# Kernel optimization log

Hardware: AMD Instinct MI355X
Metric: run time of the kernel (lower is better)

## Reference

```python
import jax, jax.numpy as jnp
import numpy as np

B, S, HID = 2, 2048, 2048
NH, NKV = 16, 4
HD = HID // NH            # 128
N_REP = NH // NKV          # 4
THETA = 10000.0
NEG = -1e9


def _rope_tables(position_ids):
    # inv_freq: [HD/2]
    inv_freq = 1.0 / (THETA ** (jnp.arange(0, HD, 2, dtype=jnp.float32) / HD))
    freqs = position_ids.astype(jnp.float32)[..., None] * inv_freq  # [B,S,HD/2]
    emb = jnp.concatenate([freqs, freqs], axis=-1)                  # [B,S,HD]
    return jnp.cos(emb), jnp.sin(emb)


def _rotate_half(x):
    return jnp.concatenate([-x[..., HD // 2:], x[..., :HD // 2]], axis=-1)


def setup_inputs() -> dict:
    key = jax.random.key(0)
    k1, k2, k3 = jax.random.split(key, 3)
    hidden_states = jax.random.normal(k1, (B, S, HID), dtype=jnp.float32)
    w_qkv = jax.random.normal(k2, (HID + 2 * NKV * HD, HID), dtype=jnp.float32) * 0.02
    w_out = jax.random.normal(k3, (HID, HID), dtype=jnp.float32) * 0.02
    causal = jnp.tril(jnp.ones((S, S), dtype=bool))
    attention_mask = jnp.where(causal, 0.0, NEG).astype(jnp.float32)
    attention_mask = jnp.broadcast_to(attention_mask[None, None], (B, 1, S, S))
    position_ids = jnp.broadcast_to(jnp.arange(S, dtype=jnp.int64), (B, S))
    return {"hidden_states": hidden_states, "w_qkv": w_qkv, "w_out": w_out,
            "attention_mask": attention_mask, "position_ids": position_ids}


def reference(hidden_states, w_qkv, w_out, attention_mask, position_ids):
    bsz, q_len, _ = hidden_states.shape
    qkv = hidden_states @ w_qkv.T                                   # [B,S,HID+2*NKV*HD]
    q, k, v = jnp.split(qkv, [HID, HID + NKV * HD], axis=-1)
    q = q.reshape(bsz, q_len, NH, HD).transpose(0, 2, 1, 3)         # [B,NH,S,HD]
    k = k.reshape(bsz, q_len, NKV, HD).transpose(0, 2, 1, 3)        # [B,NKV,S,HD]
    v = v.reshape(bsz, q_len, NKV, HD).transpose(0, 2, 1, 3)

    cos, sin = _rope_tables(position_ids)                           # [B,S,HD]
    cos, sin = cos[:, None], sin[:, None]                           # unsqueeze head dim
    q = q * cos + _rotate_half(q) * sin
    k = k * cos + _rotate_half(k) * sin

    # GQA: repeat KV heads to match query heads (repeat_kv)
    k = jnp.repeat(k, N_REP, axis=1)                                # [B,NH,S,HD]
    v = jnp.repeat(v, N_REP, axis=1)

    scale = 1.0 / jnp.sqrt(jnp.float32(HD))
    scores = jnp.einsum('bhqd,bhkd->bhqk', q, k) * scale
    scores = scores + attention_mask                                # [B,NH,S,S]
    attn = jax.nn.softmax(scores.astype(jnp.float32), axis=-1).astype(q.dtype)
    out = jnp.einsum('bhqk,bhkd->bhqd', attn, v)                    # [B,NH,S,HD]
    out = out.transpose(0, 2, 1, 3).reshape(bsz, q_len, HID)
    return out @ w_out.T
```

## Files before the change

kernel.cpp:

```cpp
#include <hip/hip_runtime.h>
#include <hip/hip_bf16.h>
#include <math.h>

#define S_LEN   2048
#define HIDDEN  2048
#define NHEADS  16
#define NKVH    4
#define HDIM    128

typedef short  short8  __attribute__((ext_vector_type(8)));
typedef float  floatx4 __attribute__((ext_vector_type(4)));
typedef __hip_bfloat16 bf16;

__device__ inline void async_copy16(const void* g, void* l) {
  __builtin_amdgcn_global_load_lds((__attribute__((address_space(1))) void*)(g),
                                   (__attribute__((address_space(3))) void*)(l),
                                   16, 0, 0);
}

__device__ inline unsigned short cvt1(float x) {
  bf16 t = __float2bfloat16(x);
  return *reinterpret_cast<unsigned short*>(&t);
}
__device__ inline float us2f(unsigned short u) {
  unsigned int v = ((unsigned int)u) << 16;
  return *reinterpret_cast<float*>(&v);
}

#define N8_H  1048576
#define N8_WQ  786432
#define N8_WO  524288
__global__ __launch_bounds__(256) void cvt_all(const float* __restrict__ h,
                                               const float* __restrict__ wq,
                                               const float* __restrict__ wo,
                                               unsigned short* __restrict__ dst) {
  const int i = blockIdx.x * 256 + threadIdx.x;
  if (i >= N8_H + N8_WQ + N8_WO) return;
  const float* src; int j;
  if (i < N8_H)              { src = h;  j = i; }
  else if (i < N8_H + N8_WQ) { src = wq; j = i - N8_H; }
  else                       { src = wo; j = i - N8_H - N8_WQ; }
  const float4 a = reinterpret_cast<const float4*>(src)[j * 2];
  const float4 b = reinterpret_cast<const float4*>(src)[j * 2 + 1];
  unsigned short o[8] = {cvt1(a.x), cvt1(a.y), cvt1(a.z), cvt1(a.w),
                         cvt1(b.x), cvt1(b.y), cvt1(b.z), cvt1(b.w)};
  *reinterpret_cast<short8*>(dst + (size_t)i * 8) = *reinterpret_cast<short8*>(o);
}

template<int MODE>
__global__ __launch_bounds__(512, 2) void gemm8(const bf16* __restrict__ A,
                                                const bf16* __restrict__ B,
                                                bf16* __restrict__ qbuf,
                                                bf16* __restrict__ kbuf,
                                                bf16* __restrict__ vtbuf,
                                                float* __restrict__ Cout)
{
  constexpr int K      = 2048;
  constexpr int BM     = (MODE == 0) ? 256 : 128;
  constexpr int BN     = 256;
  constexpr int MF     = BM / 32;
  constexpr int AI     = BM / 128;
  constexpr int ABYTES = BM * 64;
  constexpr int SLOT   = (BM + BN) * 64;
  constexpr int NSTEP  = K / 32;

  __shared__ __align__(16) unsigned short smem[SLOT * 4 / 2];
  char* smb = (char*)smem;

  const int bn = blockIdx.x, bm = blockIdx.y;
  const int t = threadIdx.x, w = t >> 6, lane = t & 63;
  const int m16 = lane & 15, quad = lane >> 4;
  const int wmr = (w >> 2) * (BM / 2);
  const int wn  = w & 3;

  int bcol[4];
#pragma unroll
  for (int ni = 0; ni < 4; ++ni)
    bcol[ni] = (MODE == 0)
             ? ((wn >> 1) * 128 + (wn & 1) * 32 + (ni & 1) * 16 + (ni >> 1) * 64)
             : (wn * 64 + ni * 16);

  int afo[MF], bfo[4];
#pragma unroll
  for (int mf = 0; mf < MF; ++mf) {
    const int r = wmr + mf * 16 + m16;
    afo[mf] = r * 64 + ((quad ^ ((r >> 1) & 3)) << 4);
  }
#pragma unroll
  for (int ni = 0; ni < 4; ++ni) {
    const int r = bcol[ni] + m16;
    bfo[ni] = ABYTES + r * 64 + ((quad ^ ((r >> 1) & 3)) << 4);
  }

  const bf16* srcA[AI]; int dstA[AI];
#pragma unroll
  for (int j = 0; j < AI; ++j) {
    const int ci  = w * AI + j;
    const int row = ci * 16 + (lane >> 2);
    const int sl  = (lane & 3) ^ ((row >> 1) & 3);
    srcA[j] = A + (size_t)(bm * BM + row) * K + sl * 8;
    dstA[j] = ci * 1024;
  }
  const bf16* srcB[2]; int dstB[2];
#pragma unroll
  for (int j = 0; j < 2; ++j) {
    const int ci  = w * 2 + j;
    const int row = ci * 16 + (lane >> 2);
    const int sl  = (lane & 3) ^ ((row >> 1) & 3);
    srcB[j] = B + (size_t)(bn * BN + row) * K + sl * 8;
    dstB[j] = ABYTES + ci * 1024;
  }

  auto stage = [&](int step, int slotbyte) {
#pragma unroll
    for (int j = 0; j < AI; ++j)
      async_copy16(srcA[j] + step * 32, smb + slotbyte + dstA[j]);
#pragma unroll
    for (int j = 0; j < 2; ++j)
      async_copy16(srcB[j] + step * 32, smb + slotbyte + dstB[j]);
  };

  const floatx4 zf = {0.f, 0.f, 0.f, 0.f};
  floatx4 acc[MF][4];
#pragma unroll
  for (int mf = 0; mf < MF; ++mf)
#pragma unroll
    for (int ni = 0; ni < 4; ++ni) acc[mf][ni] = zf;

  stage(0, 0); stage(1, SLOT); stage(2, 2 * SLOT);

#pragma unroll 4
  for (int s = 0; s < NSTEP; ++s) {
    __builtin_amdgcn_sched_barrier(0);
    if constexpr (MODE == 0) asm volatile("s_waitcnt vmcnt(8)" ::: "memory");
    else                     asm volatile("s_waitcnt vmcnt(6)" ::: "memory");
    __builtin_amdgcn_s_barrier();
    __builtin_amdgcn_sched_barrier(0);
    const int sb  = (s & 3) * SLOT;
    const int ns  = (s + 3) & (NSTEP - 1);
    const int nsb = ((s + 3) & 3) * SLOT;
    if constexpr (MODE == 0) {
      short8 bfr[4], afA[4];
#pragma unroll
      for (int ni = 0; ni < 4; ++ni)
        bfr[ni] = *reinterpret_cast<const short8*>(smb + sb + bfo[ni]);
#pragma unroll
      for (int mf = 0; mf < 4; ++mf)
        afA[mf] = *reinterpret_cast<const short8*>(smb + sb + afo[mf]);
#pragma unroll
      for (int j = 0; j < AI; ++j)
        async_copy16(srcA[j] + ns * 32, smb + nsb + dstA[j]);
      asm volatile("s_waitcnt lgkmcnt(0)" ::: "memory");
      __builtin_amdgcn_sched_barrier(0);
      __builtin_amdgcn_s_setprio(1);
#pragma unroll
      for (int mf = 0; mf < 4; ++mf)
#pragma unroll
        for (int ni = 0; ni < 4; ++ni)
          acc[mf][ni] = __builtin_amdgcn_mfma_f32_16x16x32_bf16(afA[mf], bfr[ni], acc[mf][ni], 0, 0, 0);
      __builtin_amdgcn_s_setprio(0);
      __builtin_amdgcn_s_barrier();
      short8 afB[4];
#pragma unroll
      for (int mf = 0; mf < 4; ++mf)
        afB[mf] = *reinterpret_cast<const short8*>(smb + sb + afo[4 + mf]);
#pragma unroll
      for (int j = 0; j < 2; ++j)
        async_copy16(srcB[j] + ns * 32, smb + nsb + dstB[j]);
      asm volatile("s_waitcnt lgkmcnt(0)" ::: "memory");
      __builtin_amdgcn_sched_barrier(0);
      __builtin_amdgcn_s_setprio(1);
#pragma unroll
      for (int mf = 0; mf < 4; ++mf)
#pragma unroll
        for (int ni = 0; ni < 4; ++ni)
          acc[4 + mf][ni] = __builtin_amdgcn_mfma_f32_16x16x32_bf16(afB[mf], bfr[ni], acc[4 + mf][ni], 0, 0, 0);
      __builtin_amdgcn_s_setprio(0);
    } else {
      short8 af[MF], bfr[4];
#pragma unroll
      for (int mf = 0; mf < MF; ++mf)
        af[mf] = *reinterpret_cast<const short8*>(smb + sb + afo[mf]);
#pragma unroll
      for (int ni = 0; ni < 4; ++ni)
        bfr[ni] = *reinterpret_cast<const short8*>(smb + sb + bfo[ni]);
      stage(ns, nsb);
      __builtin_amdgcn_s_setprio(1);
#pragma unroll
      for (int mf = 0; mf < MF; ++mf)
#pragma unroll
        for (int ni = 0; ni < 4; ++ni)
          acc[mf][ni] = __builtin_amdgcn_mfma_f32_16x16x32_bf16(af[mf], bfr[ni], acc[mf][ni], 0, 0, 0);
      __builtin_amdgcn_s_setprio(0);
    }
  }
  __builtin_amdgcn_s_waitcnt(0);

  if constexpr (MODE == 1) {
#pragma unroll
    for (int mf = 0; mf < MF; ++mf)
#pragma unroll
      for (int ni = 0; ni < 4; ++ni) {
        const int row0 = bm * BM + wmr + mf * 16 + quad * 4;
        const int col  = bn * BN + bcol[ni] + m16;
#pragma unroll
        for (int r = 0; r < 4; ++r)
          Cout[(size_t)(row0 + r) * HIDDEN + col] = acc[mf][ni][r];
      }
  } else {
    const int colbase = bn * BN;
    if (colbase < HIDDEN + NKVH * HDIM) {
      const bool isQ = (colbase < HIDDEN);
      const float post = isQ ? 0.08838834764831845f : 1.0f;
      float invf[2];
#pragma unroll
      for (int p = 0; p < 2; ++p)
        invf[p] = exp2f((float)((wn & 1) * 32 + p * 16 + m16) * -0.2076205059f);
#pragma unroll
      for (int mf = 0; mf < MF; ++mf) {
        const int row0 = bm * BM + wmr + mf * 16 + quad * 4;
#pragma unroll
        for (int r = 0; r < 4; ++r) {
          const int m = row0 + r;
          const int b = m >> 11, s = m & 2047;
          float sn[2], cs[2];
          __sincosf((float)s * invf[0], &sn[0], &cs[0]);
          __sincosf((float)s * invf[1], &sn[1], &cs[1]);
#pragma unroll
          for (int ni = 0; ni < 4; ++ni) {
            const int p = ni & 1;
            const float v  = acc[mf][ni][r];
            const float v2 = acc[mf][ni ^ 2][r];
            const float rot = ((ni < 2) ? (v * cs[p] - v2 * sn[p])
                                        : (v * cs[p] + v2 * sn[p])) * post;
            const int col = colbase + bcol[ni] + m16;
            if (isQ) {
              const int hh = col >> 7, d = col & 127;
              qbuf[(((size_t)(b * NHEADS + hh)) * S_LEN + s) * HDIM + d] = __float2bfloat16(rot);
            } else {
              const int nn = col - HIDDEN; const int hh = nn >> 7, d = nn & 127;
              kbuf[(((size_t)(b * NKVH + hh)) * S_LEN + s) * HDIM + d] = __float2bfloat16(rot);
            }
          }
        }
      }
    } else {
#pragma unroll
      for (int mf = 0; mf < MF; ++mf)
#pragma unroll
        for (int ni = 0; ni < 4; ++ni) {
          const int col = colbase + bcol[ni] + m16;
          const int nn = col - HIDDEN - NKVH * HDIM;
          const int hh = nn >> 7, d = nn & 127;
          const int row0 = bm * BM + wmr + mf * 16 + quad * 4;
#pragma unroll
          for (int r = 0; r < 4; ++r) {
            const int m = row0 + r;
            const int b = m >> 11, s = m & 2047;
            vtbuf[(((size_t)(b * NKVH + hh)) * HDIM + d) * S_LEN + s] =
                __float2bfloat16(acc[mf][ni][r]);
          }
        }
    }
  }
}

__global__ __launch_bounds__(256) void attn_partial(const bf16* __restrict__ qbuf,
                                                    const bf16* __restrict__ kbuf,
                                                    const bf16* __restrict__ vtbuf,
                                                    unsigned short* __restrict__ pnum,
                                                    float* __restrict__ plsum,
                                                    bf16* __restrict__ abuf)
{
  __shared__ unsigned short Ks[4][4096];
  __shared__ unsigned short Vs[4][4096];
  __shared__ unsigned short Ps[4][1280];
  const int sidx = 110 - blockIdx.x;
  int i2, c, nch;
  if (sidx < 27)      { i2 = sidx;                     c = 0;              nch = 1; }
  else if (sidx < 81) { i2 = 27 + ((sidx - 27) >> 1);  c = (sidx - 27) & 1; nch = 2; }
  else                { i2 = 54 + (sidx - 81) / 3;     c = (sidx - 81) % 3; nch = 3; }
  const int len = i2 + 1;
  const int k0 = (c * len) / nch, k1 = ((c + 1) * len) / nch;
  const int kvh = blockIdx.y, b = blockIdx.z;
  const int t = threadIdx.x, w = t >> 6, lane = t & 63;
  const int m16 = lane & 15, quad = lane >> 4;
  const int h = kvh * 4 + w;

  const bf16* Qp = qbuf + (((size_t)(b * NHEADS + h)) * S_LEN + i2 * 32 + m16) * HDIM;
  short8 qf[2][4];
#pragma unroll
  for (int T = 0; T < 2; ++T)
#pragma unroll
    for (int cc = 0; cc < 4; ++cc)
      qf[T][cc] = *reinterpret_cast<const short8*>(Qp + (size_t)T * 16 * HDIM + cc * 32 + quad * 8);

  const bf16* Kp  = kbuf  + ((size_t)(b * NKVH + kvh)) * S_LEN * HDIM;
  const bf16* Vtp = vtbuf + ((size_t)(b * NKVH + kvh)) * HDIM * S_LEN;

  const int kk = lane >> 4, cK = lane & 15;
  const int rKa = w * 8 + kk, rKb = rKa + 4;
  const int offKa = rKa * 128 + ((cK ^ (rKa & 7)) * 8);
  const int offKb = rKb * 128 + ((cK ^ (rKb & 7)) * 8);
  const int dd = lane >> 2, cV = lane & 3;
  const int dVa = w * 32 + dd, dVb = dVa + 16;
  const int offVa = dVa * 2048 + ((cV ^ ((dVa >> 1) & 3)) * 8);
  const int offVb = dVb * 2048 + ((cV ^ ((dVb >> 1) & 3)) * 8);

  const floatx4 zf = {0.f, 0.f, 0.f, 0.f};
  floatx4 oacc[2][8];
#pragma unroll
  for (int T = 0; T < 2; ++T)
#pragma unroll
    for (int d = 0; d < 8; ++d) oacc[T][d] = zf;
  floatx4 lacc[2] = {zf, zf};
  unsigned short ones_s[8] = {0x3F80,0x3F80,0x3F80,0x3F80,0x3F80,0x3F80,0x3F80,0x3F80};
  const short8 ones = *reinterpret_cast<short8*>(ones_s);

  unsigned short* Pw = &Ps[w][0];

  auto stage_tile = [&](int kt) {
    const int sl = kt & 3;
    const int ks = kt * 32;
    async_copy16(Kp + (size_t)ks * 128 + offKa, &Ks[sl][w * 1024]);
    async_copy16(Kp + (size_t)ks * 128 + offKb, &Ks[sl][w * 1024 + 512]);
    async_copy16(Vtp + ks + offVa, &Vs[sl][w * 1024]);
    async_copy16(Vtp + ks + offVb, &Vs[sl][w * 1024 + 512]);
  };

  auto qk = [&](int kt, floatx4& s00, floatx4& s01, floatx4& s10, floatx4& s11) {
    const int sl = kt & 3;
    s00 = zf; s01 = zf; s10 = zf; s11 = zf;
#pragma unroll
    for (int cc = 0; cc < 4; ++cc) {
      const int sw = ((cc * 4 + quad) ^ (m16 & 7)) * 8;
      short8 kf0 = *reinterpret_cast<const short8*>(&Ks[sl][m16 * 128 + sw]);
      short8 kf1 = *reinterpret_cast<const short8*>(&Ks[sl][(16 + m16) * 128 + sw]);
      s00 = __builtin_amdgcn_mfma_f32_16x16x32_bf16(qf[0][cc], kf0, s00, 0, 0, 0);
      s01 = __builtin_amdgcn_mfma_f32_16x16x32_bf16(qf[0][cc], kf1, s01, 0, 0, 0);
      s10 = __builtin_amdgcn_mfma_f32_16x16x32_bf16(qf[1][cc], kf0, s10, 0, 0, 0);
      s11 = __builtin_amdgcn_mfma_f32_16x16x32_bf16(qf[1][cc], kf1, s11, 0, 0, 0);
    }
  };

  auto finish = [&](int kt, const floatx4& s00, const floatx4& s01,
                    const floatx4& s10, const floatx4& s11) {
    const int sl = kt & 3;
    const int ks = kt * 32;
#pragma unroll
    for (int T = 0; T < 2; ++T) {
      const floatx4& sa = T ? s10 : s00;
      const floatx4& sb = T ? s11 : s01;
#pragma unroll
      for (int r = 0; r < 4; ++r) {
        const int row = i2 * 32 + T * 16 + quad * 4 + r;
        const float p0 = (ks + m16      > row) ? 0.f : __expf(sa[r]);
        const float p1 = (ks + 16 + m16 > row) ? 0.f : __expf(sb[r]);
        Pw[(T * 16 + quad * 4 + r) * 40 + m16]      = cvt1(p0);
        Pw[(T * 16 + quad * 4 + r) * 40 + 16 + m16] = cvt1(p1);
      }
    }
    const short8 pa0 = *reinterpret_cast<const short8*>(&Pw[m16 * 40 + quad * 8]);
    const short8 pa1 = *reinterpret_cast<const short8*>(&Pw[(16 + m16) * 40 + quad * 8]);
    lacc[0] = __builtin_amdgcn_mfma_f32_16x16x32_bf16(pa0, ones, lacc[0], 0, 0, 0);
    lacc[1] = __builtin_amdgcn_mfma_f32_16x16x32_bf16(pa1, ones, lacc[1], 0, 0, 0);
#pragma unroll
    for (int dt = 0; dt < 8; ++dt) {
      short8 vfr = *reinterpret_cast<const short8*>(
          &Vs[sl][(dt * 16 + m16) * 32 + ((quad ^ ((m16 >> 1) & 3)) * 8)]);
      oacc[0][dt] = __builtin_amdgcn_mfma_f32_16x16x32_bf16(pa0, vfr, oacc[0][dt], 0, 0, 0);
      oacc[1][dt] = __builtin_amdgcn_mfma_f32_16x16x32_bf16(pa1, vfr, oacc[1][dt], 0, 0, 0);
    }
  };

  stage_tile(k0);
  if (k0 + 1 < k1) stage_tile(k0 + 1);
  __syncthreads();
  floatx4 a00, a01, a10, a11, b00, b01, b10, b11;
  qk(k0, a00, a01, a10, a11);

  int ki = k0 + 1;
  for (; ki + 1 < k1; ki += 2) {
    stage_tile(ki + 1);
    qk(ki, b00, b01, b10, b11);
    finish(ki - 1, a00, a01, a10, a11);
    __syncthreads();
    if (ki + 2 < k1) stage_tile(ki + 2);
    qk(ki + 1, a00, a01, a10, a11);
    finish(ki, b00, b01, b10, b11);
    __syncthreads();
  }
  if (ki < k1) {
    qk(ki, b00, b01, b10, b11);
    finish(ki - 1, a00, a01, a10, a11);
    finish(ki, b00, b01, b10, b11);
  } else {
    finish(ki - 1, a00, a01, a10, a11);
  }

  if (nch == 1) {
#pragma unroll
    for (int T = 0; T < 2; ++T) {
      float invl[4];
#pragma unroll
      for (int r = 0; r < 4; ++r) invl[r] = 1.0f / lacc[T][r];
      bf16* op = abuf + (((size_t)b * S_LEN + i2 * 32 + T * 16 + quad * 4) * NHEADS + h) * HDIM + m16;
#pragma unroll
      for (int dt = 0; dt < 8; ++dt)
#pragma unroll
        for (int r = 0; r < 4; ++r)
          op[(size_t)r * NHEADS * HDIM + dt * 16] = __float2bfloat16(oacc[T][dt][r] * invl[r]);
    }
  } else {
    const int b0 = (i2 < 54) ? (27 + 2 * (i2 - 27)) : (81 + 3 * (i2 - 54));
    const int slot = (b * NHEADS + h) * 111 + b0 + c;
    unsigned short* np = pnum + (size_t)slot * 4096;
#pragma unroll
    for (int T = 0; T < 2; ++T)
#pragma unroll
      for (int dt = 0; dt < 8; ++dt)
#pragma unroll
        for (int r = 0; r < 4; ++r)
          np[(T * 16 + quad * 4 + r) * 128 + dt * 16 + m16] = cvt1(oacc[T][dt][r]);
    if (m16 == 0) {
#pragma unroll
      for (int T = 0; T < 2; ++T)
#pragma unroll
        for (int r = 0; r < 4; ++r)
          plsum[slot * 32 + T * 16 + quad * 4 + r] = lacc[T][r];
    }
  }
}

__global__ __launch_bounds__(256) void attn_combine(const unsigned short* __restrict__ pnum,
                                                    const float* __restrict__ plsum,
                                                    bf16* __restrict__ abuf)
{
  const int i = 54 + blockIdx.x;
  const int h = blockIdx.y, b = blockIdx.z;
  const int i2 = i >> 1, lr0 = (i & 1) * 16;
  const int t = threadIdx.x, row16 = t >> 4, c0 = (t & 15) * 8;
  const int lr = lr0 + row16;
  const int nch = (i2 < 54) ? 2 : 3;
  const int b0  = (i2 < 54) ? (27 + 2 * (i2 - 27)) : (81 + 3 * (i2 - 54));
  const int hb = (b * NHEADS + h) * 111 + b0;
  float acc[8] = {0.f,0.f,0.f,0.f,0.f,0.f,0.f,0.f};
  float lsum = 0.f;
  for (int c = 0; c < nch; ++c) {
    const unsigned short* np = pnum + (size_t)(hb + c) * 4096 + lr * 128 + c0;
    const short8 v = *reinterpret_cast<const short8*>(np);
#pragma unroll
    for (int j = 0; j < 8; ++j) acc[j] += us2f(((unsigned short*)&v)[j]);
    lsum += plsum[(hb + c) * 32 + lr];
  }
  const float invl = 1.0f / lsum;
  unsigned short o[8];
#pragma unroll
  for (int j = 0; j < 8; ++j) o[j] = cvt1(acc[j] * invl);
  *reinterpret_cast<short8*>(abuf + (((size_t)b * S_LEN + i * 16 + row16) * NHEADS + h) * HDIM + c0)
      = *reinterpret_cast<short8*>(o);
}

extern "C" void kernel_launch(void* const* d_in, const int* in_sizes, int n_in,
                              void* d_out, int out_size, void* d_ws, size_t ws_size,
                              hipStream_t stream) {
  const float* hidden_f = (const float*)d_in[0];
  const float* wqkv_f   = (const float*)d_in[1];
  const float* wout_f   = (const float*)d_in[2];
  float* out = (float*)d_out;

  char* ws = (char*)d_ws;
  bf16* hbf    = (bf16*)(ws);
  bf16* wqkvbf = (bf16*)(ws + 16777216);
  bf16* woutbf = (bf16*)(ws + 29360128);
  bf16* qbuf   = (bf16*)(ws + 37748736);
  bf16* kbuf   = (bf16*)(ws + 54525952);
  bf16* vtbuf  = (bf16*)(ws + 58720256);
  bf16* abuf   = (bf16*)(ws + 62914560);
  unsigned short* pnum = (unsigned short*)(ws);
  float* plsum = (float*)(ws + 79691776);

  cvt_all<<<9216, 256, 0, stream>>>(hidden_f, wqkv_f, wout_f, (unsigned short*)ws);

  gemm8<0><<<dim3(12, 16), 512, 0, stream>>>(hbf, wqkvbf, qbuf, kbuf, vtbuf, nullptr);
  attn_partial<<<dim3(111, 4, 2), 256, 0, stream>>>(qbuf, kbuf, vtbuf, pnum, plsum, abuf);
  attn_combine<<<dim3(74, 16, 2), 256, 0, stream>>>(pnum, plsum, abuf);
  gemm8<1><<<dim3(8, 32), 512, 0, stream>>>(abuf, woutbf, nullptr, nullptr, nullptr, out);
}
```

Baseline: 303.5 us.

## Use 32x32x16 MFMA in attention and keep P in registers via lane shuffles

```diff
diff --git a/kernel.cpp b/kernel.cpp
--- a/kernel.cpp
+++ b/kernel.cpp
@@ -8,8 +8,10 @@
 #define NKVH    4
 #define HDIM    128
 
-typedef short  short8  __attribute__((ext_vector_type(8)));
-typedef float  floatx4 __attribute__((ext_vector_type(4)));
+typedef short  short8   __attribute__((ext_vector_type(8)));
+typedef float  floatx4  __attribute__((ext_vector_type(4)));
+typedef float  floatx16 __attribute__((ext_vector_type(16)));
+typedef int    intx4    __attribute__((ext_vector_type(4)));
 typedef __hip_bfloat16 bf16;
 
 __device__ inline void async_copy16(const void* g, void* l) {
@@ -274,7 +276,6 @@
 {
   __shared__ unsigned short Ks[4][4096];
   __shared__ unsigned short Vs[4][4096];
-  __shared__ unsigned short Ps[4][1280];
   const int sidx = 110 - blockIdx.x;
   int i2, c, nch;
   if (sidx < 27)      { i2 = sidx;                     c = 0;              nch = 1; }
@@ -284,40 +285,32 @@
   const int k0 = (c * len) / nch, k1 = ((c + 1) * len) / nch;
   const int kvh = blockIdx.y, b = blockIdx.z;
   const int t = threadIdx.x, w = t >> 6, lane = t & 63;
-  const int m16 = lane & 15, quad = lane >> 4;
+  const int l31 = lane & 31, hi = lane >> 5;
   const int h = kvh * 4 + w;
 
-  const bf16* Qp = qbuf + (((size_t)(b * NHEADS + h)) * S_LEN + i2 * 32 + m16) * HDIM;
-  short8 qf[2][4];
-#pragma unroll
-  for (int T = 0; T < 2; ++T)
-#pragma unroll
-    for (int cc = 0; cc < 4; ++cc)
-      qf[T][cc] = *reinterpret_cast<const short8*>(Qp + (size_t)T * 16 * HDIM + cc * 32 + quad * 8);
+  const bf16* Qp = qbuf + (((size_t)(b * NHEADS + h)) * S_LEN + i2 * 32 + l31) * HDIM;
+  short8 qf[8];
+#pragma unroll
+  for (int cc = 0; cc < 8; ++cc)
+    qf[cc] = *reinterpret_cast<const short8*>(Qp + cc * 16 + hi * 8);
 
   const bf16* Kp  = kbuf  + ((size_t)(b * NKVH + kvh)) * S_LEN * HDIM;
   const bf16* Vtp = vtbuf + ((size_t)(b * NKVH + kvh)) * HDIM * S_LEN;
 
   const int kk = lane >> 4, cK = lane & 15;
   const int rKa = w * 8 + kk, rKb = rKa + 4;
-  const int offKa = rKa * 128 + ((cK ^ (rKa & 7)) * 8);
-  const int offKb = rKb * 128 + ((cK ^ (rKb & 7)) * 8);
+  const int offKa = rKa * 128 + ((cK ^ (rKa & 15)) * 8);
+  const int offKb = rKb * 128 + ((cK ^ (rKb & 15)) * 8);
   const int dd = lane >> 2, cV = lane & 3;
   const int dVa = w * 32 + dd, dVb = dVa + 16;
   const int offVa = dVa * 2048 + ((cV ^ ((dVa >> 1) & 3)) * 8);
   const int offVb = dVb * 2048 + ((cV ^ ((dVb >> 1) & 3)) * 8);
 
-  const floatx4 zf = {0.f, 0.f, 0.f, 0.f};
-  floatx4 oacc[2][8];
-#pragma unroll
-  for (int T = 0; T < 2; ++T)
-#pragma unroll
-    for (int d = 0; d < 8; ++d) oacc[T][d] = zf;
-  floatx4 lacc[2] = {zf, zf};
+  floatx16 oacc[4], lacc;
+#pragma unroll
+  for (int i = 0; i < 16; ++i) { lacc[i] = 0.f; oacc[0][i] = 0.f; oacc[1][i] = 0.f; oacc[2][i] = 0.f; oacc[3][i] = 0.f; }
   unsigned short ones_s[8] = {0x3F80,0x3F80,0x3F80,0x3F80,0x3F80,0x3F80,0x3F80,0x3F80};
   const short8 ones = *reinterpret_cast<short8*>(ones_s);
-
-  unsigned short* Pw = &Ps[w][0];
 
   auto stage_tile = [&](int kt) {
     const int sl = kt & 3;
@@ -328,106 +321,108 @@
     async_copy16(Vtp + ks + offVb, &Vs[sl][w * 1024 + 512]);
   };
 
-  auto qk = [&](int kt, floatx4& s00, floatx4& s01, floatx4& s10, floatx4& s11) {
+  auto qk = [&](int kt, floatx16& s) {
     const int sl = kt & 3;
-    s00 = zf; s01 = zf; s10 = zf; s11 = zf;
-#pragma unroll
-    for (int cc = 0; cc < 4; ++cc) {
-      const int sw = ((cc * 4 + quad) ^ (m16 & 7)) * 8;
-      short8 kf0 = *reinterpret_cast<const short8*>(&Ks[sl][m16 * 128 + sw]);
-      short8 kf1 = *reinterpret_cast<const short8*>(&Ks[sl][(16 + m16) * 128 + sw]);
-      s00 = __builtin_amdgcn_mfma_f32_16x16x32_bf16(qf[0][cc], kf0, s00, 0, 0, 0);
-      s01 = __builtin_amdgcn_mfma_f32_16x16x32_bf16(qf[0][cc], kf1, s01, 0, 0, 0);
-      s10 = __builtin_amdgcn_mfma_f32_16x16x32_bf16(qf[1][cc], kf0, s10, 0, 0, 0);
-      s11 = __builtin_amdgcn_mfma_f32_16x16x32_bf16(qf[1][cc], kf1, s11, 0, 0, 0);
+#pragma unroll
+    for (int i = 0; i < 16; ++i) s[i] = 0.f;
+#pragma unroll
+    for (int cc = 0; cc < 8; ++cc) {
+      const short8 kf = *reinterpret_cast<const short8*>(
+          &Ks[sl][l31 * 128 + (((cc * 2 + hi) ^ (l31 & 15)) * 8)]);
+      s = __builtin_amdgcn_mfma_f32_32x32x16_bf16(kf, qf[cc], s, 0, 0, 0);
     }
   };
 
-  auto finish = [&](int kt, const floatx4& s00, const floatx4& s01,
-                    const floatx4& s10, const floatx4& s11) {
+  auto finish = [&](int kt, const floatx16& s) {
     const int sl = kt & 3;
     const int ks = kt * 32;
-#pragma unroll
-    for (int T = 0; T < 2; ++T) {
-      const floatx4& sa = T ? s10 : s00;
-      const floatx4& sb = T ? s11 : s01;
-#pragma unroll
-      for (int r = 0; r < 4; ++r) {
-        const int row = i2 * 32 + T * 16 + quad * 4 + r;
-        const float p0 = (ks + m16      > row) ? 0.f : __expf(sa[r]);
-        const float p1 = (ks + 16 + m16 > row) ? 0.f : __expf(sb[r]);
-        Pw[(T * 16 + quad * 4 + r) * 40 + m16]      = cvt1(p0);
-        Pw[(T * 16 + quad * 4 + r) * 40 + 16 + m16] = cvt1(p1);
-      }
-    }
-    const short8 pa0 = *reinterpret_cast<const short8*>(&Pw[m16 * 40 + quad * 8]);
-    const short8 pa1 = *reinterpret_cast<const short8*>(&Pw[(16 + m16) * 40 + quad * 8]);
-    lacc[0] = __builtin_amdgcn_mfma_f32_16x16x32_bf16(pa0, ones, lacc[0], 0, 0, 0);
-    lacc[1] = __builtin_amdgcn_mfma_f32_16x16x32_bf16(pa1, ones, lacc[1], 0, 0, 0);
-#pragma unroll
-    for (int dt = 0; dt < 8; ++dt) {
-      short8 vfr = *reinterpret_cast<const short8*>(
-          &Vs[sl][(dt * 16 + m16) * 32 + ((quad ^ ((m16 >> 1) & 3)) * 8)]);
-      oacc[0][dt] = __builtin_amdgcn_mfma_f32_16x16x32_bf16(pa0, vfr, oacc[0][dt], 0, 0, 0);
-      oacc[1][dt] = __builtin_amdgcn_mfma_f32_16x16x32_bf16(pa1, vfr, oacc[1][dt], 0, 0, 0);
+    const int qrow = i2 * 32 + l31;
+    unsigned int cw[8];
+#pragma unroll
+    for (int tt = 0; tt < 8; ++tt) {
+      const int r0 = 2 * tt;
+      const int key0 = ks + (r0 & 3) + 8 * (r0 >> 2) + 4 * hi;
+      const float p0 = (key0     > qrow) ? 0.f : __expf(s[r0]);
+      const float p1 = (key0 + 1 > qrow) ? 0.f : __expf(s[r0 + 1]);
+      cw[tt] = ((unsigned int)cvt1(p1) << 16) | cvt1(p0);
+    }
+    unsigned int pc[8];
+#pragma unroll
+    for (int tt = 0; tt < 8; ++tt) pc[tt] = (unsigned int)__shfl_xor((int)cw[tt], 32);
+    intx4 f0, f1;
+    f0[0] = (int)(hi ? pc[2] : cw[0]); f0[1] = (int)(hi ? pc[3] : cw[1]);
+    f0[2] = (int)(hi ? cw[2] : pc[0]); f0[3] = (int)(hi ? cw[3] : pc[1]);
+    f1[0] = (int)(hi ? pc[6] : cw[4]); f1[1] = (int)(hi ? pc[7] : cw[5]);
+    f1[2] = (int)(hi ? cw[6] : pc[4]); f1[3] = (int)(hi ? cw[7] : pc[5]);
+    const short8 pf0 = __builtin_bit_cast(short8, f0);
+    const short8 pf1 = __builtin_bit_cast(short8, f1);
+    lacc = __builtin_amdgcn_mfma_f32_32x32x16_bf16(pf0, ones, lacc, 0, 0, 0);
+    lacc = __builtin_amdgcn_mfma_f32_32x32x16_bf16(pf1, ones, lacc, 0, 0, 0);
+#pragma unroll
+    for (int db = 0; db < 4; ++db) {
+      const int drow = db * 32 + l31;
+      const int xr = (drow >> 1) & 3;
+      const short8 vf0 = *reinterpret_cast<const short8*>(
+          &Vs[sl][drow * 32 + ((hi ^ xr) * 8)]);
+      oacc[db] = __builtin_amdgcn_mfma_f32_32x32x16_bf16(pf0, vf0, oacc[db], 0, 0, 0);
+      const short8 vf1 = *reinterpret_cast<const short8*>(
+          &Vs[sl][drow * 32 + (((2 + hi) ^ xr) * 8)]);
+      oacc[db] = __builtin_amdgcn_mfma_f32_32x32x16_bf16(pf1, vf1, oacc[db], 0, 0, 0);
     }
   };
 
   stage_tile(k0);
   if (k0 + 1 < k1) stage_tile(k0 + 1);
   __syncthreads();
-  floatx4 a00, a01, a10, a11, b00, b01, b10, b11;
-  qk(k0, a00, a01, a10, a11);
+  floatx16 sa, sb;
+  qk(k0, sa);
 
   int ki = k0 + 1;
   for (; ki + 1 < k1; ki += 2) {
     stage_tile(ki + 1);
-    qk(ki, b00, b01, b10, b11);
-    finish(ki - 1, a00, a01, a10, a11);
+    qk(ki, sb);
+    finish(ki - 1, sa);
     __syncthreads();
     if (ki + 2 < k1) stage_tile(ki + 2);
-    qk(ki + 1, a00, a01, a10, a11);
-    finish(ki, b00, b01, b10, b11);
+    qk(ki + 1, sa);
+    finish(ki, sb);
     __syncthreads();
   }
   if (ki < k1) {
-    qk(ki, b00, b01, b10, b11);
-    finish(ki - 1, a00, a01, a10, a11);
-    finish(ki, b00, b01, b10, b11);
+    qk(ki, sb);
+    finish(ki - 1, sa);
+    finish(ki, sb);
   } else {
-    finish(ki - 1, a00, a01, a10, a11);
+    finish(ki - 1, sa);
   }
 
   if (nch == 1) {
-#pragma unroll
-    for (int T = 0; T < 2; ++T) {
-      float invl[4];
-#pragma unroll
-      for (int r = 0; r < 4; ++r) invl[r] = 1.0f / lacc[T][r];
-      bf16* op = abuf + (((size_t)b * S_LEN + i2 * 32 + T * 16 + quad * 4) * NHEADS + h) * HDIM + m16;
-#pragma unroll
-      for (int dt = 0; dt < 8; ++dt)
-#pragma unroll
-        for (int r = 0; r < 4; ++r)
-          op[(size_t)r * NHEADS * HDIM + dt * 16] = __float2bfloat16(oacc[T][dt][r] * invl[r]);
-    }
+    float invl[16];
+#pragma unroll
+    for (int r = 0; r < 16; ++r) invl[r] = 1.0f / lacc[r];
+#pragma unroll
+    for (int db = 0; db < 4; ++db)
+#pragma unroll
+      for (int r = 0; r < 16; ++r) {
+        const int row = i2 * 32 + (r & 3) + 8 * (r >> 2) + 4 * hi;
+        abuf[(((size_t)b * S_LEN + row) * NHEADS + h) * HDIM + db * 32 + l31] =
+            __float2bfloat16(oacc[db][r] * invl[r]);
+      }
   } else {
     const int b0 = (i2 < 54) ? (27 + 2 * (i2 - 27)) : (81 + 3 * (i2 - 54));
     const int slot = (b * NHEADS + h) * 111 + b0 + c;
     unsigned short* np = pnum + (size_t)slot * 4096;
 #pragma unroll
-    for (int T = 0; T < 2; ++T)
-#pragma unroll
-      for (int dt = 0; dt < 8; ++dt)
-#pragma unroll
-        for (int r = 0; r < 4; ++r)
-          np[(T * 16 + quad * 4 + r) * 128 + dt * 16 + m16] = cvt1(oacc[T][dt][r]);
-    if (m16 == 0) {
-#pragma unroll
-      for (int T = 0; T < 2; ++T)
-#pragma unroll
-        for (int r = 0; r < 4; ++r)
-          plsum[slot * 32 + T * 16 + quad * 4 + r] = lacc[T][r];
+    for (int db = 0; db < 4; ++db)
+#pragma unroll
+      for (int r = 0; r < 16; ++r) {
+        const int row = (r & 3) + 8 * (r >> 2) + 4 * hi;
+        np[row * 128 + db * 32 + l31] = cvt1(oacc[db][r]);
+      }
+    if (l31 == 0) {
+#pragma unroll
+      for (int r = 0; r < 16; ++r)
+        plsum[slot * 32 + (r & 3) + 8 * (r >> 2) + 4 * hi] = lacc[r];
     }
   }
 }
```

New measurement: 328.3 us. +8.1%, slower.

## Stage 128-key K/V blocks per sync and rebalance split-K chunk partitioning

Applied to the files above, without the earlier changes.

```diff
diff --git a/kernel.cpp b/kernel.cpp
--- a/kernel.cpp
+++ b/kernel.cpp
@@ -272,16 +272,16 @@
                                                     float* __restrict__ plsum,
                                                     bf16* __restrict__ abuf)
 {
-  __shared__ unsigned short Ks[4][4096];
-  __shared__ unsigned short Vs[4][4096];
+  __shared__ unsigned short Ks[16384];
+  __shared__ unsigned short Vs[16384];
   __shared__ unsigned short Ps[4][1280];
-  const int sidx = 110 - blockIdx.x;
+  const int sidx = 119 - blockIdx.x;
   int i2, c, nch;
-  if (sidx < 27)      { i2 = sidx;                     c = 0;              nch = 1; }
-  else if (sidx < 81) { i2 = 27 + ((sidx - 27) >> 1);  c = (sidx - 27) & 1; nch = 2; }
-  else                { i2 = 54 + (sidx - 81) / 3;     c = (sidx - 81) % 3; nch = 3; }
-  const int len = i2 + 1;
-  const int k0 = (c * len) / nch, k1 = ((c + 1) * len) / nch;
+  if (sidx < 24)      { i2 = sidx;                          c = 0;     nch = 1; }
+  else if (sidx < 72) { const int q = sidx - 24; i2 = 24 + (q >> 1); c = q & 1; nch = 2; }
+  else                { const int q = sidx - 72; i2 = 48 + q / 3;    c = q % 3; nch = 3; }
+  const int L = (i2 >> 2) + 1;
+  const int kb0 = (c * L) / nch, kb1 = ((c + 1) * L) / nch;
   const int kvh = blockIdx.y, b = blockIdx.z;
   const int t = threadIdx.x, w = t >> 6, lane = t & 63;
   const int m16 = lane & 15, quad = lane >> 4;
@@ -298,14 +298,8 @@
   const bf16* Kp  = kbuf  + ((size_t)(b * NKVH + kvh)) * S_LEN * HDIM;
   const bf16* Vtp = vtbuf + ((size_t)(b * NKVH + kvh)) * HDIM * S_LEN;
 
-  const int kk = lane >> 4, cK = lane & 15;
-  const int rKa = w * 8 + kk, rKb = rKa + 4;
-  const int offKa = rKa * 128 + ((cK ^ (rKa & 7)) * 8);
-  const int offKb = rKb * 128 + ((cK ^ (rKb & 7)) * 8);
-  const int dd = lane >> 2, cV = lane & 3;
-  const int dVa = w * 32 + dd, dVb = dVa + 16;
-  const int offVa = dVa * 2048 + ((cV ^ ((dVa >> 1) & 3)) * 8);
-  const int offVb = dVb * 2048 + ((cV ^ ((dVb >> 1) & 3)) * 8);
+  const int ls = lane >> 4;
+  const int lc = lane & 15;
 
   const floatx4 zf = {0.f, 0.f, 0.f, 0.f};
   floatx4 oacc[2][8];
@@ -319,23 +313,24 @@
 
   unsigned short* Pw = &Ps[w][0];
 
-  auto stage_tile = [&](int kt) {
-    const int sl = kt & 3;
-    const int ks = kt * 32;
-    async_copy16(Kp + (size_t)ks * 128 + offKa, &Ks[sl][w * 1024]);
-    async_copy16(Kp + (size_t)ks * 128 + offKb, &Ks[sl][w * 1024 + 512]);
-    async_copy16(Vtp + ks + offVa, &Vs[sl][w * 1024]);
-    async_copy16(Vtp + ks + offVb, &Vs[sl][w * 1024 + 512]);
+  auto stage_tile = [&](int kb) {
+#pragma unroll
+    for (int j = 0; j < 8; ++j) {
+      const int r = w * 32 + j * 4 + ls;
+      async_copy16(Kp + ((size_t)(kb * 128 + r)) * 128 + ((lc ^ (r & 7)) * 8),
+                   &Ks[(w * 32 + j * 4) * 128]);
+      async_copy16(Vtp + (size_t)r * 2048 + kb * 128 + ((lc ^ (r & 7)) * 8),
+                   &Vs[(w * 32 + j * 4) * 128]);
+    }
   };
 
-  auto qk = [&](int kt, floatx4& s00, floatx4& s01, floatx4& s10, floatx4& s11) {
-    const int sl = kt & 3;
+  auto qk = [&](int sub, floatx4& s00, floatx4& s01, floatx4& s10, floatx4& s11) {
     s00 = zf; s01 = zf; s10 = zf; s11 = zf;
 #pragma unroll
     for (int cc = 0; cc < 4; ++cc) {
-      const int sw = ((cc * 4 + quad) ^ (m16 & 7)) * 8;
-      short8 kf0 = *reinterpret_cast<const short8*>(&Ks[sl][m16 * 128 + sw]);
-      short8 kf1 = *reinterpret_cast<const short8*>(&Ks[sl][(16 + m16) * 128 + sw]);
+      const int ch = ((cc * 4 + quad) ^ (m16 & 7)) * 8;
+      short8 kf0 = *reinterpret_cast<const short8*>(&Ks[(sub * 32 + m16) * 128 + ch]);
+      short8 kf1 = *reinterpret_cast<const short8*>(&Ks[(sub * 32 + 16 + m16) * 128 + ch]);
       s00 = __builtin_amdgcn_mfma_f32_16x16x32_bf16(qf[0][cc], kf0, s00, 0, 0, 0);
       s01 = __builtin_amdgcn_mfma_f32_16x16x32_bf16(qf[0][cc], kf1, s01, 0, 0, 0);
       s10 = __builtin_amdgcn_mfma_f32_16x16x32_bf16(qf[1][cc], kf0, s10, 0, 0, 0);
@@ -343,10 +338,9 @@
     }
   };
 
-  auto finish = [&](int kt, const floatx4& s00, const floatx4& s01,
+  auto finish = [&](int kb, int sub, const floatx4& s00, const floatx4& s01,
                     const floatx4& s10, const floatx4& s11) {
-    const int sl = kt & 3;
-    const int ks = kt * 32;
+    const int ks = kb * 128 + sub * 32;
 #pragma unroll
     for (int T = 0; T < 2; ++T) {
       const floatx4& sa = T ? s10 : s00;
@@ -367,35 +361,35 @@
 #pragma unroll
     for (int dt = 0; dt < 8; ++dt) {
       short8 vfr = *reinterpret_cast<const short8*>(
-          &Vs[sl][(dt * 16 + m16) * 32 + ((quad ^ ((m16 >> 1) & 3)) * 8)]);
+          &Vs[(dt * 16 + m16) * 128 + (((sub * 4 + quad) ^ (m16 & 7)) * 8)]);
       oacc[0][dt] = __builtin_amdgcn_mfma_f32_16x16x32_bf16(pa0, vfr, oacc[0][dt], 0, 0, 0);
       oacc[1][dt] = __builtin_amdgcn_mfma_f32_16x16x32_bf16(pa1, vfr, oacc[1][dt], 0, 0, 0);
     }
   };
 
-  stage_tile(k0);
-  if (k0 + 1 < k1) stage_tile(k0 + 1);
-  __syncthreads();
-  floatx4 a00, a01, a10, a11, b00, b01, b10, b11;
-  qk(k0, a00, a01, a10, a11);
-
-  int ki = k0 + 1;
-  for (; ki + 1 < k1; ki += 2) {
-    stage_tile(ki + 1);
-    qk(ki, b00, b01, b10, b11);
-    finish(ki - 1, a00, a01, a10, a11);
+  for (int kb = kb0; kb < kb1; ++kb) {
     __syncthreads();
-    if (ki + 2 < k1) stage_tile(ki + 2);
-    qk(ki + 1, a00, a01, a10, a11);
-    finish(ki, b00, b01, b10, b11);
+    stage_tile(kb);
     __syncthreads();
-  }
-  if (ki < k1) {
-    qk(ki, b00, b01, b10, b11);
-    finish(ki - 1, a00, a01, a10, a11);
-    finish(ki, b00, b01, b10, b11);
-  } else {
-    finish(ki - 1, a00, a01, a10, a11);
+    const int rem = i2 - 4 * kb + 1;
+    floatx4 a0, a1, a2, a3, b0, b1, b2, b3;
+    qk(0, a0, a1, a2, a3);
+    if (rem == 1) { finish(kb, 0, a0, a1, a2, a3); }
+    else {
+      qk(1, b0, b1, b2, b3);
+      finish(kb, 0, a0, a1, a2, a3);
+      if (rem == 2) { finish(kb, 1, b0, b1, b2, b3); }
+      else {
+        qk(2, a0, a1, a2, a3);
+        finish(kb, 1, b0, b1, b2, b3);
+        if (rem == 3) { finish(kb, 2, a0, a1, a2, a3); }
+        else {
+          qk(3, b0, b1, b2, b3);
+          finish(kb, 2, a0, a1, a2, a3);
+          finish(kb, 3, b0, b1, b2, b3);
+        }
+      }
+    }
   }
 
   if (nch == 1) {
@@ -412,8 +406,8 @@
           op[(size_t)r * NHEADS * HDIM + dt * 16] = __float2bfloat16(oacc[T][dt][r] * invl[r]);
     }
   } else {
-    const int b0 = (i2 < 54) ? (27 + 2 * (i2 - 27)) : (81 + 3 * (i2 - 54));
-    const int slot = (b * NHEADS + h) * 111 + b0 + c;
+    const int base = (i2 < 48) ? (i2 - 24) * 2 : 48 + (i2 - 48) * 3;
+    const int slot = (b * NHEADS + h) * 96 + base + c;
     unsigned short* np = pnum + (size_t)slot * 4096;
 #pragma unroll
     for (int T = 0; T < 2; ++T)
@@ -436,14 +430,14 @@
                                                     const float* __restrict__ plsum,
                                                     bf16* __restrict__ abuf)
 {
-  const int i = 54 + blockIdx.x;
+  const int i = blockIdx.x;
+  const int i2 = 24 + (i >> 1), lr0 = (i & 1) * 16;
   const int h = blockIdx.y, b = blockIdx.z;
-  const int i2 = i >> 1, lr0 = (i & 1) * 16;
   const int t = threadIdx.x, row16 = t >> 4, c0 = (t & 15) * 8;
   const int lr = lr0 + row16;
-  const int nch = (i2 < 54) ? 2 : 3;
-  const int b0  = (i2 < 54) ? (27 + 2 * (i2 - 27)) : (81 + 3 * (i2 - 54));
-  const int hb = (b * NHEADS + h) * 111 + b0;
+  const int nch  = (i2 < 48) ? 2 : 3;
+  const int base = (i2 < 48) ? (i2 - 24) * 2 : 48 + (i2 - 48) * 3;
+  const int hb = (b * NHEADS + h) * 96 + base;
   float acc[8] = {0.f,0.f,0.f,0.f,0.f,0.f,0.f,0.f};
   float lsum = 0.f;
   for (int c = 0; c < nch; ++c) {
@@ -457,7 +451,7 @@
   unsigned short o[8];
 #pragma unroll
   for (int j = 0; j < 8; ++j) o[j] = cvt1(acc[j] * invl);
-  *reinterpret_cast<short8*>(abuf + (((size_t)b * S_LEN + i * 16 + row16) * NHEADS + h) * HDIM + c0)
+  *reinterpret_cast<short8*>(abuf + (((size_t)b * S_LEN + i2 * 32 + lr) * NHEADS + h) * HDIM + c0)
       = *reinterpret_cast<short8*>(o);
 }
 
@@ -483,7 +477,7 @@
   cvt_all<<<9216, 256, 0, stream>>>(hidden_f, wqkv_f, wout_f, (unsigned short*)ws);
 
   gemm8<0><<<dim3(12, 16), 512, 0, stream>>>(hbf, wqkvbf, qbuf, kbuf, vtbuf, nullptr);
-  attn_partial<<<dim3(111, 4, 2), 256, 0, stream>>>(qbuf, kbuf, vtbuf, pnum, plsum, abuf);
-  attn_combine<<<dim3(74, 16, 2), 256, 0, stream>>>(pnum, plsum, abuf);
+  attn_partial<<<dim3(120, 4, 2), 256, 0, stream>>>(qbuf, kbuf, vtbuf, pnum, plsum, abuf);
+  attn_combine<<<dim3(80, 16, 2), 256, 0, stream>>>(pnum, plsum, abuf);
   gemm8<1><<<dim3(8, 32), 512, 0, stream>>>(abuf, woutbf, nullptr, nullptr, nullptr, out);
 }
```

Measured after the change: 328.1 us. +8.1%, slower.
